# Kernel optimization log

Hardware: AMD Instinct MI355X
Metric: run time of the kernel (lower is better)

## Reference

```python
import jax, jax.numpy as jnp
import numpy as np

B, S, D, H = 2, 2048, 1024, 16
DK = D // H  # 64


def setup_inputs() -> dict:
    key = jax.random.key(0)
    ks = jax.random.split(key, 8)
    sc = 1.0 / np.sqrt(D)
    return {
        "q": jax.random.normal(ks[0], (B, S, D), jnp.float32),
        "k": jax.random.normal(ks[1], (B, S, D), jnp.float32),
        "v": jax.random.normal(ks[2], (B, S, D), jnp.float32),
        "Wq": jax.random.normal(ks[3], (D, D), jnp.float32) * sc,
        "bq": jnp.zeros((D,), jnp.float32),
        "Wk": jax.random.normal(ks[4], (D, D), jnp.float32) * sc,
        "bk": jnp.zeros((D,), jnp.float32),
        "Wv": jax.random.normal(ks[5], (D, D), jnp.float32) * sc,
        "bv": jnp.zeros((D,), jnp.float32),
        "Wo": jax.random.normal(ks[6], (D, D), jnp.float32) * sc,
        "bo": jnp.zeros((D,), jnp.float32),
    }


def _heads(x, W, b):
    # torch nn.Linear: x @ W.T + b, then view(bs,-1,H,DK).transpose(1,2)
    bsz, seq, _ = x.shape
    y = x @ W.T + b
    return y.reshape(bsz, seq, H, DK).transpose(0, 2, 1, 3)  # [B,H,S,DK]


def reference(q, k, v, Wq, bq, Wk, bk, Wv, bv, Wo, bo):
    qh = _heads(q, Wq, bq)
    kh = _heads(k, Wk, bk)
    vh = _heads(v, Wv, bv)
    # scores: [B,H,S,S]; intended scale 1/sqrt(d_k) (source passes tensor k as d_k by mistake)
    scores = jnp.einsum("bhqd,bhkd->bhqk", qh, kh) / jnp.sqrt(jnp.float32(DK))
    attn = jax.nn.softmax(scores, axis=-1)  # dropout is identity in eval
    ctx = jnp.einsum("bhqk,bhkd->bhqd", attn, vh)  # [B,H,S,DK]
    concat = ctx.transpose(0, 2, 1, 3).reshape(-1, H * DK)  # [B*S, D] (source flattens batch+seq)
    return concat @ Wo.T + bo
```

## Files before the change

### kernel.cpp

```cpp
#include <hip/hip_runtime.h>

typedef __attribute__((ext_vector_type(4))) float f32x4;
typedef __attribute__((ext_vector_type(8))) short short8;
typedef __attribute__((ext_vector_type(4))) unsigned short u16x4;
typedef __attribute__((ext_vector_type(2))) unsigned u32x2;
typedef __attribute__((ext_vector_type(4))) unsigned u32x4;

#define DEV static __device__ __forceinline__

#define BSZ 2
#define SEQ 2048
#define DMODEL 1024
#define NH 16
#define DKH 64
#define MROWS (BSZ*SEQ)
#define HEAD_ELEMS (BSZ*NH*SEQ*DKH)
#define WMAT_ELEMS (DMODEL*DMODEL)
#define QSCALE 0.18033688011111374f

DEV unsigned short f2bf(float f) {
    unsigned u = __builtin_bit_cast(unsigned, f);
    u += 0x7FFFu + ((u >> 16) & 1u);
    return (unsigned short)(u >> 16);
}

DEV unsigned cvtpk(float a, float b) {
    unsigned r;
    asm("v_cvt_pk_bf16_f32 %0, %1, %2" : "=v"(r) : "v"(a), "v"(b));
    return r;
}

DEV float fexp2(float x) {
#if __has_builtin(__builtin_amdgcn_exp2f)
    return __builtin_amdgcn_exp2f(x);
#else
    float r;
    asm("v_exp_f32 %0, %1\n\ts_nop 0" : "=v"(r) : "v"(x));
    return r;
#endif
}

DEV void gload16(const void* g, void* l) {
    __builtin_amdgcn_global_load_lds(
        (const __attribute__((address_space(1))) void*)g,
        (__attribute__((address_space(3))) void*)l, 16, 0, 0);
}

DEV void cfence() { asm volatile("" ::: "memory"); }

__global__ __launch_bounds__(256) void convall_kernel(
    const float* __restrict__ q, const float* __restrict__ k,
    const float* __restrict__ v,
    const float* __restrict__ Wq, const float* __restrict__ Wk,
    const float* __restrict__ Wv, const float* __restrict__ Wo,
    unsigned short* __restrict__ abf, unsigned short* __restrict__ wbf)
{
    const int z = blockIdx.y;
    const int i = (blockIdx.x * 256 + threadIdx.x) * 8;
    const float* src;
    unsigned short* dst;
    if (z < 3) {
        src = ((z == 0) ? q : (z == 1) ? k : v) + i;
        dst = abf + (size_t)z * HEAD_ELEMS + i;
    } else {
        const int mi = i >> 20;
        const int off = i & (WMAT_ELEMS - 1);
        src = ((mi == 0) ? Wq : (mi == 1) ? Wk : (mi == 2) ? Wv : Wo) + off;
        dst = wbf + i;
    }
    f32x4 a = *(const f32x4*)(src);
    f32x4 b = *(const f32x4*)(src + 4);
    u32x4 o;
    o[0] = cvtpk(a[0], a[1]); o[1] = cvtpk(a[2], a[3]);
    o[2] = cvtpk(b[0], b[1]); o[3] = cvtpk(b[2], b[3]);
    *(u32x4*)(dst) = o;
}

__global__ __launch_bounds__(256) void wconv_kernel(
    const float* __restrict__ Wq, const float* __restrict__ Wk,
    const float* __restrict__ Wv, const float* __restrict__ Wo,
    unsigned short* __restrict__ dst)
{
    const int z = blockIdx.y;
    const float* src = (z == 0) ? Wq : (z == 1) ? Wk : (z == 2) ? Wv : Wo;
    const int i = (blockIdx.x * 256 + threadIdx.x) * 4;
    f32x4 v = *(const f32x4*)(src + i);
    u16x4 o;
    o[0] = f2bf(v[0]); o[1] = f2bf(v[1]); o[2] = f2bf(v[2]); o[3] = f2bf(v[3]);
    *(u16x4*)(dst + (size_t)z * WMAT_ELEMS + i) = o;
}

__global__ __launch_bounds__(256) void aconv_kernel(
    const float* __restrict__ src, unsigned short* __restrict__ dst)
{
    const int i = (blockIdx.x * 256 + threadIdx.x) * 8;
    f32x4 a = *(const f32x4*)(src + i);
    f32x4 b = *(const f32x4*)(src + i + 4);
    u32x4 o;
    o[0] = cvtpk(a[0], a[1]); o[1] = cvtpk(a[2], a[3]);
    o[2] = cvtpk(b[0], b[1]); o[3] = cvtpk(b[2], b[3]);
    *(u32x4*)(dst + i) = o;
}

__global__ __launch_bounds__(256, 3) void proj_gemm_kernel(
    const unsigned short* __restrict__ Aq, const unsigned short* __restrict__ Ak,
    const unsigned short* __restrict__ Av,
    const unsigned short* __restrict__ Wbf,
    const float* __restrict__ bq, const float* __restrict__ bk, const float* __restrict__ bvv,
    unsigned short* __restrict__ heads, int zbase)
{
    const int z = zbase + blockIdx.z;
    const unsigned short* A = (z == 0) ? Aq : (z == 1) ? Ak : Av;
    const float* bias = (z == 0) ? bq : (z == 1) ? bk : bvv;
    const unsigned short* W = Wbf + (size_t)z * WMAT_ELEMS;
    unsigned short* outp = heads + (size_t)z * HEAD_ELEMS;

    __shared__ __align__(16) unsigned short As[128 * 64];
    __shared__ __align__(16) unsigned short Bs[128 * 64];

    const int tid = threadIdx.x;
    const int lane = tid & 63;
    const int w = tid >> 6;
    const int wr = w >> 1, wc = w & 1;
    const int l15 = lane & 15, l4 = lane >> 4;
    const int m0 = blockIdx.x * 128, n0 = blockIdx.y * 128;

    f32x4 acc[4][4];
    #pragma unroll
    for (int i = 0; i < 4; i++)
        #pragma unroll
        for (int j = 0; j < 4; j++) acc[i][j] = (f32x4){0.f, 0.f, 0.f, 0.f};

    const int srow = w * 8 + (lane >> 3);
    const int ssrc = ((lane & 7) ^ (srow & 7)) * 8;
    const unsigned short* ga = A + (size_t)(m0 + srow) * DMODEL + ssrc;
    const unsigned short* gb = W + (size_t)(n0 + srow) * DMODEL + ssrc;

    for (int k0 = 0; k0 < DMODEL; k0 += 64) {
        __syncthreads();
        #pragma unroll
        for (int c = 0; c < 4; c++) {
            gload16(ga + (size_t)c * 32 * DMODEL + k0, As + (c * 4 + w) * 512);
            gload16(gb + (size_t)c * 32 * DMODEL + k0, Bs + (c * 4 + w) * 512);
        }
        __syncthreads();

        short8 af[2][4], bf[2][4];
        #pragma unroll
        for (int mi = 0; mi < 4; mi++) {
            const int r = wr * 64 + mi * 16 + l15;
            const int x = r & 7;
            const char* base = (const char*)As + r * 128;
            af[0][mi] = *(const short8*)(base + ((l4 ^ x) << 4));
            af[1][mi] = *(const short8*)(base + (((4 + l4) ^ x) << 4));
        }
        #pragma unroll
        for (int ni = 0; ni < 4; ni++) {
            const int r = wc * 64 + ni * 16 + l15;
            const int x = r & 7;
            const char* base = (const char*)Bs + r * 128;
            bf[0][ni] = *(const short8*)(base + ((l4 ^ x) << 4));
            bf[1][ni] = *(const short8*)(base + (((4 + l4) ^ x) << 4));
        }

        __builtin_amdgcn_s_setprio(1);
        #pragma unroll
        for (int ks = 0; ks < 2; ks++)
            #pragma unroll
            for (int mi = 0; mi < 4; mi++)
                #pragma unroll
                for (int ni = 0; ni < 4; ni++)
                    acc[mi][ni] = __builtin_amdgcn_mfma_f32_16x16x32_bf16(
                        af[ks][mi], bf[ks][ni], acc[mi][ni], 0, 0, 0);
        __builtin_amdgcn_s_setprio(0);
    }

    if (z < 2) {
        const float sc = (z == 0) ? QSCALE : 1.0f;
        #pragma unroll
        for (int ni = 0; ni < 4; ni++) {
            const int n = n0 + wc * 64 + ni * 16 + l15;
            const float bn = bias[n];
            const int h = n >> 6, dk = n & 63;
            #pragma unroll
            for (int mi = 0; mi < 4; mi++) {
                #pragma unroll
                for (int r = 0; r < 4; r++) {
                    const int m = m0 + wr * 64 + mi * 16 + l4 * 4 + r;
                    const int b = m >> 11, s = m & 2047;
                    outp[((size_t)((b * NH + h) * SEQ) + s) * DKH + dk] =
                        f2bf((acc[mi][ni][r] + bn) * sc);
                }
            }
        }
    } else {
        #pragma unroll
        for (int ni = 0; ni < 4; ni++) {
            const int n = n0 + wc * 64 + ni * 16 + l15;
            const float bn = bias[n];
            const int h = n >> 6, dk = n & 63;
            #pragma unroll
            for (int mi = 0; mi < 4; mi++) {
                const int m = m0 + wr * 64 + mi * 16 + l4 * 4;
                const int b = m >> 11, s = m & 2047;
                float v0 = acc[mi][ni][0] + bn, v1 = acc[mi][ni][1] + bn;
                float v2 = acc[mi][ni][2] + bn, v3 = acc[mi][ni][3] + bn;
                u32x2 pk; pk[0] = cvtpk(v0, v1); pk[1] = cvtpk(v2, v3);
                *(u32x2*)(outp + ((size_t)((b * NH + h) * DKH + dk)) * SEQ + s) = pk;
            }
        }
    }
}

#define KVB 64
#define NTILES (SEQ/KVB)

__global__ __launch_bounds__(256, 2) void attn_kernel(
    const unsigned short* __restrict__ Qh, const unsigned short* __restrict__ Kh,
    const unsigned short* __restrict__ Vtg, unsigned short* __restrict__ Ctx)
{
    __shared__ __align__(16) char lds[49152];

    const int tid = threadIdx.x;
    const int lane = tid & 63, w = tid >> 6;
    const int l15 = lane & 15, l4 = lane >> 4;

    const int bid = blockIdx.x;
    const int bh = (bid & 7) * 4 + (bid >> 7);
    const int qt = (bid >> 3) & 15;
    const int q0 = qt * 128;

    const unsigned short* Qp = Qh + (size_t)bh * (SEQ * DKH);
    const unsigned short* Kp = Kh + (size_t)bh * (SEQ * DKH);
    const unsigned short* Vp = Vtg + (size_t)bh * (SEQ * DKH);
    char* Pw = lds + 32768 + w * 4096;

    const unsigned short* qrow = Qp + (size_t)(q0 + w * 32 + l15) * DKH + l4 * 8;
    const short8 qf0h0 = *(const short8*)(qrow);
    const short8 qf1h0 = *(const short8*)(qrow + 32);
    const short8 qf0h1 = *(const short8*)(qrow + 16 * DKH);
    const short8 qf1h1 = *(const short8*)(qrow + 16 * DKH + 32);

    const int srow = tid >> 3;
    const int sseg = ((tid & 7) ^ (srow & 7)) * 8;
    const unsigned short* kg = Kp + (size_t)srow * DKH + sseg;
    const unsigned short* vg = Vp + (size_t)srow * SEQ + sseg;

    float lsum0 = 0.f, lsum1 = 0.f;
    f32x4 o0[4], o1[4];
    #pragma unroll
    for (int d = 0; d < 4; d++) {
        o0[d] = (f32x4){0.f, 0.f, 0.f, 0.f};
        o1[d] = (f32x4){0.f, 0.f, 0.f, 0.f};
    }

    const int fb = l15 * 128 + ((l4 * 16) ^ ((l15 & 7) << 4));
    const int pswz = (l15 & 7) << 4;

    gload16(kg,                              lds + w * 1024);
    gload16(kg + (size_t)32 * DKH,           lds + 4096 + w * 1024);
    gload16(vg,                      lds + 16384 + w * 1024);
    gload16(vg + (size_t)32 * SEQ,   lds + 16384 + 4096 + w * 1024);

    for (int t = 0; t < NTILES; ++t) {
        __syncthreads();
        const int cur = t & 1;

        if (t + 1 < NTILES) {
            const unsigned short* kn = kg + (size_t)(t + 1) * (KVB * DKH);
            const unsigned short* vn = vg + (t + 1) * KVB;
            char* kd = lds + (cur ^ 1) * 8192 + w * 1024;
            char* vd = lds + 16384 + (cur ^ 1) * 8192 + w * 1024;
            gload16(kn,                    kd);
            gload16(kn + (size_t)32 * DKH, kd + 4096);
            gload16(vn,                    vd);
            gload16(vn + (size_t)32 * SEQ, vd + 4096);
        }

        const char* Kb = lds + cur * 8192;
        const char* Vb = lds + 16384 + cur * 8192;

        f32x4 s0[4], s1[4];
        #pragma unroll
        for (int nf = 0; nf < 4; nf++) {
            s0[nf] = (f32x4){0.f, 0.f, 0.f, 0.f};
            s1[nf] = (f32x4){0.f, 0.f, 0.f, 0.f};
        }
        __builtin_amdgcn_s_setprio(1);
        #pragma unroll
        for (int ks = 0; ks < 2; ks++) {
            const int fo = fb ^ (ks << 6);
            #pragma unroll
            for (int nf = 0; nf < 4; nf++) {
                short8 kf = *(const short8*)(Kb + fo + nf * 2048);
                s0[nf] = __builtin_amdgcn_mfma_f32_16x16x32_bf16(
                    kf, ks ? qf1h0 : qf0h0, s0[nf], 0, 0, 0);
                s1[nf] = __builtin_amdgcn_mfma_f32_16x16x32_bf16(
                    kf, ks ? qf1h1 : qf0h1, s1[nf], 0, 0, 0);
            }
        }
        __builtin_amdgcn_s_setprio(0);

        cfence();

        float ps0 = 0.f, ps1 = 0.f;
        #pragma unroll
        for (int nf = 0; nf < 4; nf++) {
            const float a0 = fexp2(s0[nf][0]), a1 = fexp2(s0[nf][1]);
            const float a2 = fexp2(s0[nf][2]), a3 = fexp2(s0[nf][3]);
            ps0 += (a0 + a1) + (a2 + a3);
            u32x2 pk0; pk0[0] = cvtpk(a0, a1); pk0[1] = cvtpk(a2, a3);
            *(u32x2*)(Pw + l15 * 128 + ((nf * 32 + l4 * 8) ^ pswz)) = pk0;

            const float b0 = fexp2(s1[nf][0]), b1 = fexp2(s1[nf][1]);
            const float b2 = fexp2(s1[nf][2]), b3 = fexp2(s1[nf][3]);
            ps1 += (b0 + b1) + (b2 + b3);
            u32x2 pk1; pk1[0] = cvtpk(b0, b1); pk1[1] = cvtpk(b2, b3);
            *(u32x2*)(Pw + 2048 + l15 * 128 + ((nf * 32 + l4 * 8) ^ pswz)) = pk1;
        }
        ps0 += __shfl_xor(ps0, 16); ps0 += __shfl_xor(ps0, 32); lsum0 += ps0;
        ps1 += __shfl_xor(ps1, 16); ps1 += __shfl_xor(ps1, 32); lsum1 += ps1;

        cfence();

        __builtin_amdgcn_s_setprio(1);
        #pragma unroll
        for (int ks = 0; ks < 2; ks++) {
            const int po = (ks * 64 + l4 * 16) ^ pswz;
            short8 pa0 = *(const short8*)(Pw + l15 * 128 + po);
            short8 pa1 = *(const short8*)(Pw + 2048 + l15 * 128 + po);
            const int fo = fb ^ (ks << 6);
            #pragma unroll
            for (int d = 0; d < 4; d++) {
                short8 vb = *(const short8*)(Vb + fo + d * 2048);
                o0[d] = __builtin_amdgcn_mfma_f32_16x16x32_bf16(pa0, vb, o0[d], 0, 0, 0);
                o1[d] = __builtin_amdgcn_mfma_f32_16x16x32_bf16(pa1, vb, o1[d], 0, 0, 0);
            }
        }
        __builtin_amdgcn_s_setprio(0);

        cfence();
    }

    const int b = bh >> 4, h = bh & 15;
    {
        const float linv = 1.f / lsum0;
        #pragma unroll
        for (int r = 0; r < 4; r++) {
            const float lr = __shfl(linv, l4 * 4 + r);
            const int sq = q0 + w * 32 + l4 * 4 + r;
            const size_t base = ((size_t)(b * SEQ + sq)) * DMODEL + h * DKH;
            #pragma unroll
            for (int d = 0; d < 4; d++)
                Ctx[base + d * 16 + l15] = f2bf(o0[d][r] * lr);
        }
    }
    {
        const float linv = 1.f / lsum1;
        #pragma unroll
        for (int r = 0; r < 4; r++) {
            const float lr = __shfl(linv, l4 * 4 + r);
            const int sq = q0 + w * 32 + 16 + l4 * 4 + r;
            const size_t base = ((size_t)(b * SEQ + sq)) * DMODEL + h * DKH;
            #pragma unroll
            for (int d = 0; d < 4; d++)
                Ctx[base + d * 16 + l15] = f2bf(o1[d][r] * lr);
        }
    }
}

__global__ __launch_bounds__(256, 3) void out_gemm_kernel(
    const unsigned short* __restrict__ Ctx, const unsigned short* __restrict__ Wobf,
    const float* __restrict__ bo, float* __restrict__ outp)
{
    __shared__ __align__(16) unsigned short As[128 * 64];
    __shared__ __align__(16) unsigned short Bs[128 * 64];

    const int tid = threadIdx.x;
    const int lane = tid & 63;
    const int w = tid >> 6;
    const int wr = w >> 1, wc = w & 1;
    const int l15 = lane & 15, l4 = lane >> 4;
    const int m0 = blockIdx.x * 128, n0 = blockIdx.y * 128;

    f32x4 acc[4][4];
    #pragma unroll
    for (int i = 0; i < 4; i++)
        #pragma unroll
        for (int j = 0; j < 4; j++) acc[i][j] = (f32x4){0.f, 0.f, 0.f, 0.f};

    const int srow = w * 8 + (lane >> 3);
    const int ssrc = ((lane & 7) ^ (srow & 7)) * 8;
    const unsigned short* ga = Ctx + (size_t)(m0 + srow) * DMODEL + ssrc;
    const unsigned short* gb = Wobf + (size_t)(n0 + srow) * DMODEL + ssrc;

    for (int k0 = 0; k0 < DMODEL; k0 += 64) {
        __syncthreads();
        #pragma unroll
        for (int c = 0; c < 4; c++) {
            gload16(ga + (size_t)c * 32 * DMODEL + k0, As + (c * 4 + w) * 512);
            gload16(gb + (size_t)c * 32 * DMODEL + k0, Bs + (c * 4 + w) * 512);
        }
        __syncthreads();

        short8 af[2][4], bf[2][4];
        #pragma unroll
        for (int mi = 0; mi < 4; mi++) {
            const int r = wr * 64 + mi * 16 + l15;
            const int x = r & 7;
            const char* base = (const char*)As + r * 128;
            af[0][mi] = *(const short8*)(base + ((l4 ^ x) << 4));
            af[1][mi] = *(const short8*)(base + (((4 + l4) ^ x) << 4));
        }
        #pragma unroll
        for (int ni = 0; ni < 4; ni++) {
            const int r = wc * 64 + ni * 16 + l15;
            const int x = r & 7;
            const char* base = (const char*)Bs + r * 128;
            bf[0][ni] = *(const short8*)(base + ((l4 ^ x) << 4));
            bf[1][ni] = *(const short8*)(base + (((4 + l4) ^ x) << 4));
        }

        __builtin_amdgcn_s_setprio(1);
        #pragma unroll
        for (int ks = 0; ks < 2; ks++)
            #pragma unroll
            for (int mi = 0; mi < 4; mi++)
                #pragma unroll
                for (int ni = 0; ni < 4; ni++)
                    acc[mi][ni] = __builtin_amdgcn_mfma_f32_16x16x32_bf16(
                        af[ks][mi], bf[ks][ni], acc[mi][ni], 0, 0, 0);
        __builtin_amdgcn_s_setprio(0);
    }

    #pragma unroll
    for (int ni = 0; ni < 4; ni++) {
        const int n = n0 + wc * 64 + ni * 16 + l15;
        const float bn = bo[n];
        #pragma unroll
        for (int mi = 0; mi < 4; mi++) {
            #pragma unroll
            for (int r = 0; r < 4; r++) {
                const int m = m0 + wr * 64 + mi * 16 + l4 * 4 + r;
                outp[(size_t)m * DMODEL + n] = acc[mi][ni][r] + bn;
            }
        }
    }
}

extern "C" void kernel_launch(void* const* d_in, const int* in_sizes, int n_in,
                              void* d_out, int out_size, void* d_ws, size_t ws_size,
                              hipStream_t stream)
{
    (void)in_sizes; (void)n_in; (void)out_size;
    const float* q  = (const float*)d_in[0];
    const float* k  = (const float*)d_in[1];
    const float* v  = (const float*)d_in[2];
    const float* Wq = (const float*)d_in[3];
    const float* bq = (const float*)d_in[4];
    const float* Wk = (const float*)d_in[5];
    const float* bk = (const float*)d_in[6];
    const float* Wv = (const float*)d_in[7];
    const float* bv = (const float*)d_in[8];
    const float* Wo = (const float*)d_in[9];
    const float* bo = (const float*)d_in[10];
    float* outp = (float*)d_out;

    unsigned short* ws  = (unsigned short*)d_ws;
    unsigned short* Wbf = ws;

    const size_t BIG_NEED = (size_t)(4u * WMAT_ELEMS + 6u * HEAD_ELEMS) * 2u;

    if (ws_size >= BIG_NEED) {
        unsigned short* qbf = ws + 4u * WMAT_ELEMS;
        unsigned short* kbf = qbf + HEAD_ELEMS;
        unsigned short* vbf = kbf + HEAD_ELEMS;
        unsigned short* Qh  = vbf + HEAD_ELEMS;
        unsigned short* Kh  = Qh + HEAD_ELEMS;
        unsigned short* Vt  = Kh + HEAD_ELEMS;
        unsigned short* Ctx = qbf;

        hipLaunchKernelGGL(convall_kernel, dim3(2048, 4), dim3(256), 0, stream,
                           q, k, v, Wq, Wk, Wv, Wo, qbf, Wbf);
        hipLaunchKernelGGL(proj_gemm_kernel, dim3(32, 8, 3), dim3(256), 0, stream,
                           qbf, kbf, vbf, Wbf, bq, bk, bv, Qh, 0);
        hipLaunchKernelGGL(attn_kernel, dim3(512), dim3(256), 0, stream,
                           Qh, Kh, Vt, Ctx);
        hipLaunchKernelGGL(out_gemm_kernel, dim3(32, 8), dim3(256), 0, stream,
                           Ctx, Wbf + 3u * WMAT_ELEMS, bo, outp);
    } else {
        unsigned short* Abf = ws + 4u * WMAT_ELEMS;
        unsigned short* Qh  = Abf + HEAD_ELEMS;
        unsigned short* Kh  = Qh + HEAD_ELEMS;
        unsigned short* Vt  = Kh + HEAD_ELEMS;
        unsigned short* Ctx = Abf;

        hipLaunchKernelGGL(wconv_kernel, dim3(1024, 4), dim3(256), 0, stream,
                           Wq, Wk, Wv, Wo, Wbf);
        const float* srcs[3] = {q, k, v};
        for (int z = 0; z < 3; z++) {
            hipLaunchKernelGGL(aconv_kernel, dim3(2048), dim3(256), 0, stream, srcs[z], Abf);
            hipLaunchKernelGGL(proj_gemm_kernel, dim3(32, 8, 1), dim3(256), 0, stream,
                               Abf, Abf, Abf, Wbf, bq, bk, bv, Qh, z);
        }
        hipLaunchKernelGGL(attn_kernel, dim3(512), dim3(256), 0, stream,
                           Qh, Kh, Vt, Ctx);
        hipLaunchKernelGGL(out_gemm_kernel, dim3(32, 8), dim3(256), 0, stream,
                           Ctx, Wbf + 3u * WMAT_ELEMS, bo, outp);
    }
}
```

Before: 108.3 us.

## Software-pipeline attention: overlap next tile's QK^T with current softmax and PV

Restructures the attention main loop so that QK^T for tile i+1 is computed before softmax and PV for tile i, using two sets of score registers that alternate. V gets a triple-buffered LDS ring while K stays double-buffered, and global loads are issued two tiles ahead. The aim is to let MFMA work from the next tile overlap the exp/convert/LDS-write phase and reduce stalls between stages. The cost is more registers for the extra score arrays and 8 KB more LDS (57344 bytes per block), which could hurt occupancy at 2 blocks per CU.

```diff
diff --git a/kernel.cpp b/kernel.cpp
--- a/kernel.cpp
+++ b/kernel.cpp
@@ -214,12 +214,14 @@
 
 #define KVB 64
 #define NTILES (SEQ/KVB)
+#define VBASE 16384
+#define PBASE 40960
 
 __global__ __launch_bounds__(256, 2) void attn_kernel(
     const unsigned short* __restrict__ Qh, const unsigned short* __restrict__ Kh,
     const unsigned short* __restrict__ Vtg, unsigned short* __restrict__ Ctx)
 {
-    __shared__ __align__(16) char lds[49152];
+    __shared__ __align__(16) char lds[57344];
 
     const int tid = threadIdx.x;
     const int lane = tid & 63, w = tid >> 6;
@@ -233,7 +235,7 @@
     const unsigned short* Qp = Qh + (size_t)bh * (SEQ * DKH);
     const unsigned short* Kp = Kh + (size_t)bh * (SEQ * DKH);
     const unsigned short* Vp = Vtg + (size_t)bh * (SEQ * DKH);
-    char* Pw = lds + 32768 + w * 4096;
+    char* Pw = lds + PBASE + w * 4096;
 
     const unsigned short* qrow = Qp + (size_t)(q0 + w * 32 + l15) * DKH + l4 * 8;
     const short8 qf0h0 = *(const short8*)(qrow);
@@ -257,90 +259,109 @@
     const int fb = l15 * 128 + ((l4 * 16) ^ ((l15 & 7) << 4));
     const int pswz = (l15 & 7) << 4;
 
-    gload16(kg,                              lds + w * 1024);
-    gload16(kg + (size_t)32 * DKH,           lds + 4096 + w * 1024);
-    gload16(vg,                      lds + 16384 + w * 1024);
-    gload16(vg + (size_t)32 * SEQ,   lds + 16384 + 4096 + w * 1024);
-
-    for (int t = 0; t < NTILES; ++t) {
+#define STAGE(T, KOFF, VOFF) do {                                            \
+        const unsigned short* kn_ = kg + (size_t)(T) * (KVB * DKH);          \
+        const unsigned short* vn_ = vg + (T) * KVB;                          \
+        char* kd_ = lds + (KOFF) + w * 1024;                                 \
+        char* vd_ = lds + VBASE + (VOFF) + w * 1024;                         \
+        gload16(kn_, kd_);                                                   \
+        gload16(kn_ + (size_t)32 * DKH, kd_ + 4096);                         \
+        gload16(vn_, vd_);                                                   \
+        gload16(vn_ + (size_t)32 * SEQ, vd_ + 4096);                         \
+    } while (0)
+
+#define QKSTEP(S0, S1, KOFF) do {                                            \
+        const char* Kb_ = lds + (KOFF);                                      \
+        _Pragma("unroll")                                                    \
+        for (int nf = 0; nf < 4; nf++) {                                     \
+            S0[nf] = (f32x4){0.f, 0.f, 0.f, 0.f};                            \
+            S1[nf] = (f32x4){0.f, 0.f, 0.f, 0.f};                            \
+        }                                                                    \
+        __builtin_amdgcn_s_setprio(1);                                       \
+        _Pragma("unroll")                                                    \
+        for (int ks = 0; ks < 2; ks++) {                                     \
+            const int fo_ = fb ^ (ks << 6);                                  \
+            _Pragma("unroll")                                                \
+            for (int nf = 0; nf < 4; nf++) {                                 \
+                short8 kf_ = *(const short8*)(Kb_ + fo_ + nf * 2048);        \
+                S0[nf] = __builtin_amdgcn_mfma_f32_16x16x32_bf16(            \
+                    kf_, ks ? qf1h0 : qf0h0, S0[nf], 0, 0, 0);               \
+                S1[nf] = __builtin_amdgcn_mfma_f32_16x16x32_bf16(            \
+                    kf_, ks ? qf1h1 : qf0h1, S1[nf], 0, 0, 0);               \
+            }                                                                \
+        }                                                                    \
+        __builtin_amdgcn_s_setprio(0);                                       \
+    } while (0)
+
+#define SMPV(S0, S1, VOFF) do {                                              \
+        cfence();                                                            \
+        float ps0_ = 0.f, ps1_ = 0.f;                                        \
+        _Pragma("unroll")                                                    \
+        for (int nf = 0; nf < 4; nf++) {                                     \
+            const float a0_ = fexp2(S0[nf][0]), a1_ = fexp2(S0[nf][1]);      \
+            const float a2_ = fexp2(S0[nf][2]), a3_ = fexp2(S0[nf][3]);      \
+            ps0_ += (a0_ + a1_) + (a2_ + a3_);                               \
+            u32x2 pk0_; pk0_[0] = cvtpk(a0_, a1_); pk0_[1] = cvtpk(a2_, a3_);\
+            *(u32x2*)(Pw + l15 * 128 + ((nf * 32 + l4 * 8) ^ pswz)) = pk0_;  \
+            const float b0_ = fexp2(S1[nf][0]), b1_ = fexp2(S1[nf][1]);      \
+            const float b2_ = fexp2(S1[nf][2]), b3_ = fexp2(S1[nf][3]);      \
+            ps1_ += (b0_ + b1_) + (b2_ + b3_);                               \
+            u32x2 pk1_; pk1_[0] = cvtpk(b0_, b1_); pk1_[1] = cvtpk(b2_, b3_);\
+            *(u32x2*)(Pw + 2048 + l15 * 128 + ((nf * 32 + l4 * 8) ^ pswz)) = pk1_; \
+        }                                                                    \
+        ps0_ += __shfl_xor(ps0_, 16); ps0_ += __shfl_xor(ps0_, 32);          \
+        lsum0 += ps0_;                                                       \
+        ps1_ += __shfl_xor(ps1_, 16); ps1_ += __shfl_xor(ps1_, 32);          \
+        lsum1 += ps1_;                                                       \
+        cfence();                                                            \
+        const char* Vb_ = lds + VBASE + (VOFF);                              \
+        __builtin_amdgcn_s_setprio(1);                                       \
+        _Pragma("unroll")                                                    \
+        for (int ks = 0; ks < 2; ks++) {                                     \
+            const int po_ = (ks * 64 + l4 * 16) ^ pswz;                      \
+            short8 pa0_ = *(const short8*)(Pw + l15 * 128 + po_);            \
+            short8 pa1_ = *(const short8*)(Pw + 2048 + l15 * 128 + po_);     \
+            const int fo_ = fb ^ (ks << 6);                                  \
+            _Pragma("unroll")                                                \
+            for (int d = 0; d < 4; d++) {                                    \
+                short8 vb_ = *(const short8*)(Vb_ + fo_ + d * 2048);         \
+                o0[d] = __builtin_amdgcn_mfma_f32_16x16x32_bf16(             \
+                    pa0_, vb_, o0[d], 0, 0, 0);                              \
+                o1[d] = __builtin_amdgcn_mfma_f32_16x16x32_bf16(             \
+                    pa1_, vb_, o1[d], 0, 0, 0);                              \
+            }                                                                \
+        }                                                                    \
+        __builtin_amdgcn_s_setprio(0);                                       \
+        cfence();                                                            \
+    } while (0)
+
+    f32x4 sA0[4], sA1[4], sB0[4], sB1[4];
+
+    STAGE(0, 0, 0);
+    __syncthreads();
+    STAGE(1, 8192, 8192);
+    QKSTEP(sA0, sA1, 0);
+
+    int vr = 0;
+    int vs = 16384;
+    for (int i = 0; i < NTILES - 1; ++i) {
         __syncthreads();
-        const int cur = t & 1;
-
-        if (t + 1 < NTILES) {
-            const unsigned short* kn = kg + (size_t)(t + 1) * (KVB * DKH);
-            const unsigned short* vn = vg + (t + 1) * KVB;
-            char* kd = lds + (cur ^ 1) * 8192 + w * 1024;
-            char* vd = lds + 16384 + (cur ^ 1) * 8192 + w * 1024;
-            gload16(kn,                    kd);
-            gload16(kn + (size_t)32 * DKH, kd + 4096);
-            gload16(vn,                    vd);
-            gload16(vn + (size_t)32 * SEQ, vd + 4096);
-        }
-
-        const char* Kb = lds + cur * 8192;
-        const char* Vb = lds + 16384 + cur * 8192;
-
-        f32x4 s0[4], s1[4];
-        #pragma unroll
-        for (int nf = 0; nf < 4; nf++) {
-            s0[nf] = (f32x4){0.f, 0.f, 0.f, 0.f};
-            s1[nf] = (f32x4){0.f, 0.f, 0.f, 0.f};
-        }
-        __builtin_amdgcn_s_setprio(1);
-        #pragma unroll
-        for (int ks = 0; ks < 2; ks++) {
-            const int fo = fb ^ (ks << 6);
-            #pragma unroll
-            for (int nf = 0; nf < 4; nf++) {
-                short8 kf = *(const short8*)(Kb + fo + nf * 2048);
-                s0[nf] = __builtin_amdgcn_mfma_f32_16x16x32_bf16(
-                    kf, ks ? qf1h0 : qf0h0, s0[nf], 0, 0, 0);
-                s1[nf] = __builtin_amdgcn_mfma_f32_16x16x32_bf16(
-                    kf, ks ? qf1h1 : qf0h1, s1[nf], 0, 0, 0);
-            }
-        }
-        __builtin_amdgcn_s_setprio(0);
-
-        cfence();
-
-        float ps0 = 0.f, ps1 = 0.f;
-        #pragma unroll
-        for (int nf = 0; nf < 4; nf++) {
-            const float a0 = fexp2(s0[nf][0]), a1 = fexp2(s0[nf][1]);
-            const float a2 = fexp2(s0[nf][2]), a3 = fexp2(s0[nf][3]);
-            ps0 += (a0 + a1) + (a2 + a3);
-            u32x2 pk0; pk0[0] = cvtpk(a0, a1); pk0[1] = cvtpk(a2, a3);
-            *(u32x2*)(Pw + l15 * 128 + ((nf * 32 + l4 * 8) ^ pswz)) = pk0;
-
-            const float b0 = fexp2(s1[nf][0]), b1 = fexp2(s1[nf][1]);
-            const float b2 = fexp2(s1[nf][2]), b3 = fexp2(s1[nf][3]);
-            ps1 += (b0 + b1) + (b2 + b3);
-            u32x2 pk1; pk1[0] = cvtpk(b0, b1); pk1[1] = cvtpk(b2, b3);
-            *(u32x2*)(Pw + 2048 + l15 * 128 + ((nf * 32 + l4 * 8) ^ pswz)) = pk1;
-        }
-        ps0 += __shfl_xor(ps0, 16); ps0 += __shfl_xor(ps0, 32); lsum0 += ps0;
-        ps1 += __shfl_xor(ps1, 16); ps1 += __shfl_xor(ps1, 32); lsum1 += ps1;
-
-        cfence();
-
-        __builtin_amdgcn_s_setprio(1);
-        #pragma unroll
-        for (int ks = 0; ks < 2; ks++) {
-            const int po = (ks * 64 + l4 * 16) ^ pswz;
-            short8 pa0 = *(const short8*)(Pw + l15 * 128 + po);
-            short8 pa1 = *(const short8*)(Pw + 2048 + l15 * 128 + po);
-            const int fo = fb ^ (ks << 6);
-            #pragma unroll
-            for (int d = 0; d < 4; d++) {
-                short8 vb = *(const short8*)(Vb + fo + d * 2048);
-                o0[d] = __builtin_amdgcn_mfma_f32_16x16x32_bf16(pa0, vb, o0[d], 0, 0, 0);
-                o1[d] = __builtin_amdgcn_mfma_f32_16x16x32_bf16(pa1, vb, o1[d], 0, 0, 0);
-            }
-        }
-        __builtin_amdgcn_s_setprio(0);
-
-        cfence();
-    }
+        if (i + 2 < NTILES) STAGE(i + 2, (i & 1) * 8192, vs);
+        if (i & 1) {
+            QKSTEP(sA0, sA1, ((i + 1) & 1) * 8192);
+            SMPV(sB0, sB1, vr);
+        } else {
+            QKSTEP(sB0, sB1, ((i + 1) & 1) * 8192);
+            SMPV(sA0, sA1, vr);
+        }
+        vr += 8192; if (vr == 24576) vr = 0;
+        vs += 8192; if (vs == 24576) vs = 0;
+    }
+    SMPV(sB0, sB1, vr);
+
+#undef STAGE
+#undef QKSTEP
+#undef SMPV
 
     const int b = bh >> 4, h = bh & 15;
     {
```

After: 115.3 us. +6.5%, slower.
